# Performance work log

Hardware: AMD Instinct MI355X
Metric: run time of the kernel (lower is better)

The kernel has to match this reference:

```python
import jax, jax.numpy as jnp
import numpy as np

DIM = 1024
HEADS = 16
WINDOW = 5
B, S = 2, 2048
EPS = 1e-5


def setup_inputs() -> dict:
    key = jax.random.key(0)
    ks = jax.random.split(key, 12)
    d = DIM
    sc = lambda n: 1.0 / np.sqrt(n)
    return {
        "x": jax.random.normal(ks[0], (B, S, d), dtype=jnp.float32),
        "w_in": jax.random.normal(ks[1], (3 * d, d), dtype=jnp.float32) * sc(d),
        "b_in": jnp.zeros((3 * d,), dtype=jnp.float32),
        "w_out": jax.random.normal(ks[2], (d, d), dtype=jnp.float32) * sc(d),
        "b_out": jnp.zeros((d,), dtype=jnp.float32),
        "ln1_g": jnp.ones((d,), dtype=jnp.float32),
        "ln1_b": jnp.zeros((d,), dtype=jnp.float32),
        "ln2_g": jnp.ones((d,), dtype=jnp.float32),
        "ln2_b": jnp.zeros((d,), dtype=jnp.float32),
        "w1": jax.random.normal(ks[3], (4 * d, d), dtype=jnp.float32) * sc(d),
        "b1": jnp.zeros((4 * d,), dtype=jnp.float32),
        "w2": jax.random.normal(ks[4], (d, 4 * d), dtype=jnp.float32) * sc(4 * d),
        "b2": jnp.zeros((d,), dtype=jnp.float32),
    }


def _layernorm(x, g, b):
    mu = jnp.mean(x, axis=-1, keepdims=True)
    var = jnp.mean((x - mu) ** 2, axis=-1, keepdims=True)
    return (x - mu) * jax.lax.rsqrt(var + EPS) * g + b


def reference(x, w_in, b_in, w_out, b_out, ln1_g, ln1_b, ln2_g, ln2_b, w1, b1, w2, b2):
    Bq, Sq, d = x.shape
    hd = d // HEADS
    # in-projection (torch MHA: qkv = x @ W_in^T + b_in)
    qkv = jnp.einsum('bsd,ed->bse', x, w_in) + b_in  # [B,S,3d]
    q, k, v = jnp.split(qkv, 3, axis=-1)
    q = q.reshape(Bq, Sq, HEADS, hd)
    k = k.reshape(Bq, Sq, HEADS, hd)
    v = v.reshape(Bq, Sq, HEADS, hd)
    scale = 1.0 / np.sqrt(hd)
    scores = jnp.einsum('bqhd,bkhd->bhqk', q, k) * scale  # [B,H,S,S]
    # local causal mask: row i attends to j in [i-window+1, i]
    i = jnp.arange(Sq)[:, None]
    j = jnp.arange(Sq)[None, :]
    allowed = (j <= i) & (j > i - WINDOW)
    scores = jnp.where(allowed, scores, jnp.float32(-jnp.inf))
    probs = jax.nn.softmax(scores, axis=-1)
    attn = jnp.einsum('bhqk,bkhd->bqhd', probs, v).reshape(Bq, Sq, d)
    attn = jnp.einsum('bsd,ed->bse', attn, w_out) + b_out
    x1 = _layernorm(x + attn, ln1_g, ln1_b)
    h = jax.nn.gelu(jnp.einsum('bsd,ed->bse', x1, w1) + b1, approximate=False)
    mlp = jnp.einsum('bse,de->bsd', h, w2) + b2
    return _layernorm(x1 + mlp, ln2_g, ln2_b)
```

## Files before the change

### kernel.cpp

```cpp
#include <hip/hip_runtime.h>
#include <hip/hip_bf16.h>
#include <math.h>

typedef __hip_bfloat16 bf16;
typedef __attribute__((ext_vector_type(8))) short bf16x8;
typedef __attribute__((ext_vector_type(4))) float f32x4;

#define GPTR(p) ((const __attribute__((address_space(1))) void*)(p))
#define LPTR(p) ((__attribute__((address_space(3))) void*)(p))

__device__ __forceinline__ float b2f(short s) {
  unsigned int u = ((unsigned int)(unsigned short)s) << 16;
  float f; __builtin_memcpy(&f, &u, 4); return f;
}

__global__ __launch_bounds__(256) void cvt_all(
    const float* __restrict__ x,    const float* __restrict__ w_in,
    const float* __restrict__ w_out,const float* __restrict__ w1,
    const float* __restrict__ w2,
    bf16* __restrict__ xb,   bf16* __restrict__ winb, bf16* __restrict__ woutb,
    bf16* __restrict__ w1b,  bf16* __restrict__ w2b)
{
  const int b = blockIdx.x;
  const float* in; bf16* out; int base;
  if      (b <  4096) { in = x;     out = xb;    base = 0; }
  else if (b <  7168) { in = w_in;  out = winb;  base = 4096; }
  else if (b <  8192) { in = w_out; out = woutb; base = 7168; }
  else if (b < 12288) { in = w1;    out = w1b;   base = 8192; }
  else                { in = w2;    out = w2b;   base = 12288; }
  const int i = ((b - base) * 256 + threadIdx.x) * 4;
  const float4 f = *(const float4*)(in + i);
  ushort4 u;
  u.x = __bfloat16_as_ushort(__float2bfloat16(f.x));
  u.y = __bfloat16_as_ushort(__float2bfloat16(f.y));
  u.z = __bfloat16_as_ushort(__float2bfloat16(f.z));
  u.w = __bfloat16_as_ushort(__float2bfloat16(f.w));
  *(ushort4*)(out + i) = u;
}

__device__ __forceinline__ float gelu_fast(float v) {
  const float u  = 1.5957691216f * (v + 0.044715f * v * v * v);
  const float e  = __expf(u);
  return v * e / (e + 1.0f);
}

template<int GELU, int RESID>
__global__ __launch_bounds__(256, 4) void gemm_bt(
    const bf16* __restrict__ A, int lda,
    const bf16* __restrict__ B, int ldb,
    const float* __restrict__ bias,
    const void* __restrict__ Rv, int ldr,
    bf16* __restrict__ C, int ldc, long czstride,
    int M, int N, int kchunk)
{
  __shared__ __align__(16) bf16 As[128 * 64];
  __shared__ __align__(16) bf16 Bs[128 * 64];

  const int t    = threadIdx.x;
  const int lane = t & 63;
  const int w    = t >> 6;
  const int wm   = w >> 1;
  const int wn   = w & 1;
  const int lr   = lane & 15;
  const int lq   = lane >> 4;
  const int m0   = blockIdx.y * 128;
  const int n0   = blockIdx.x * 128;
  const int kz   = blockIdx.z;

  A += (size_t)kz * kchunk;
  B += (size_t)kz * kchunk;
  C += (size_t)kz * czstride;

  f32x4 acc[4][4];
  #pragma unroll
  for (int mi = 0; mi < 4; ++mi)
    #pragma unroll
    for (int ni = 0; ni < 4; ++ni)
      acc[mi][ni] = (f32x4){0.f, 0.f, 0.f, 0.f};

  const int wbase = (t & ~63) * 8;

  for (int k0 = 0; k0 < kchunk; k0 += 64) {
    #pragma unroll
    for (int it = 0; it < 4; ++it) {
      const int c    = it * 256 + t;
      const int row  = c >> 3;
      const int csw  = ((c & 7) ^ (row & 7)) << 3;
      const bf16* ga = A + (size_t)(m0 + row) * lda + k0 + csw;
      const bf16* gb = B + (size_t)(n0 + row) * ldb + k0 + csw;
      __builtin_amdgcn_global_load_lds(GPTR(ga), LPTR(&As[it * 2048 + wbase]), 16, 0, 0);
      __builtin_amdgcn_global_load_lds(GPTR(gb), LPTR(&Bs[it * 2048 + wbase]), 16, 0, 0);
    }
    __syncthreads();

    #pragma unroll
    for (int ks = 0; ks < 2; ++ks) {
      const int swz = (((ks * 4 + lq) ^ (lr & 7)) << 3);
      bf16x8 af[4], bfr[4];
      #pragma unroll
      for (int mi = 0; mi < 4; ++mi)
        af[mi] = *(const bf16x8*)&As[(wm * 64 + mi * 16 + lr) * 64 + swz];
      #pragma unroll
      for (int ni = 0; ni < 4; ++ni)
        bfr[ni] = *(const bf16x8*)&Bs[(wn * 64 + ni * 16 + lr) * 64 + swz];
      #pragma unroll
      for (int mi = 0; mi < 4; ++mi)
        #pragma unroll
        for (int ni = 0; ni < 4; ++ni)
          acc[mi][ni] = __builtin_amdgcn_mfma_f32_16x16x32_bf16(af[mi], bfr[ni], acc[mi][ni], 0, 0, 0);
    }
    __syncthreads();
  }

  #pragma unroll
  for (int ni = 0; ni < 4; ++ni) {
    const int col = n0 + wn * 64 + ni * 16 + lr;
    const float bv = bias ? bias[col] : 0.f;
    #pragma unroll
    for (int mi = 0; mi < 4; ++mi) {
      const int rowb = m0 + wm * 64 + mi * 16 + lq * 4;
      #pragma unroll
      for (int i = 0; i < 4; ++i) {
        float v = acc[mi][ni][i] + bv;
        if (GELU) v = gelu_fast(v);
        if (RESID == 1) v += ((const float*)Rv)[(size_t)(rowb + i) * ldr + col];
        if (RESID == 2) v += __bfloat162float(((const bf16*)Rv)[(size_t)(rowb + i) * ldr + col]);
        C[(size_t)(rowb + i) * ldc + col] = __float2bfloat16(v);
      }
    }
  }
}

__global__ __launch_bounds__(256) void attn_win(bf16* __restrict__ qkv)
{
  const int lane = threadIdx.x & 63;
  const int tk   = blockIdx.x * 4 + (threadIdx.x >> 6);
  const int s    = tk & 2047;
  const int doff = (lane >> 2) * 64 + (lane & 3) * 16;

  const size_t row = (size_t)tk * 3072;

  bf16x8 qa = *(const bf16x8*)&qkv[row + doff];
  bf16x8 qb = *(const bf16x8*)&qkv[row + doff + 8];
  float qf[16];
  #pragma unroll
  for (int e = 0; e < 8; ++e) { qf[e] = b2f(qa[e]); qf[8 + e] = b2f(qb[e]); }

  const int W = (s + 1 < 5) ? (s + 1) : 5;
  float p[5];
  #pragma unroll
  for (int j = 0; j < 5; ++j) {
    const int jc = (j < W) ? j : 0;
    const size_t kr = row - (size_t)jc * 3072 + 1024;
    bf16x8 ka = *(const bf16x8*)&qkv[kr + doff];
    bf16x8 kb = *(const bf16x8*)&qkv[kr + doff + 8];
    float d = 0.f;
    #pragma unroll
    for (int e = 0; e < 8; ++e) d += qf[e] * b2f(ka[e]);
    #pragma unroll
    for (int e = 0; e < 8; ++e) d += qf[8 + e] * b2f(kb[e]);
    d += __shfl_xor(d, 1);
    d += __shfl_xor(d, 2);
    p[j] = (j < W) ? d * 0.125f : -1e30f;
  }

  float mx = fmaxf(fmaxf(fmaxf(p[0], p[1]), fmaxf(p[2], p[3])), p[4]);
  float sum = 0.f;
  #pragma unroll
  for (int j = 0; j < 5; ++j) { p[j] = __expf(p[j] - mx); sum += p[j]; }
  const float inv = 1.f / sum;

  float o[16];
  #pragma unroll
  for (int e = 0; e < 16; ++e) o[e] = 0.f;
  #pragma unroll
  for (int j = 0; j < 5; ++j) {
    const int jc = (j < W) ? j : 0;
    const size_t vr = row - (size_t)jc * 3072 + 2048;
    bf16x8 va = *(const bf16x8*)&qkv[vr + doff];
    bf16x8 vb = *(const bf16x8*)&qkv[vr + doff + 8];
    #pragma unroll
    for (int e = 0; e < 8; ++e) { o[e] += p[j] * b2f(va[e]); o[8 + e] += p[j] * b2f(vb[e]); }
  }

  bf16x8 oa, ob;
  #pragma unroll
  for (int e = 0; e < 8; ++e) {
    oa[e] = (short)__bfloat16_as_ushort(__float2bfloat16(o[e] * inv));
    ob[e] = (short)__bfloat16_as_ushort(__float2bfloat16(o[8 + e] * inv));
  }
  *(bf16x8*)&qkv[row + doff]     = oa;
  *(bf16x8*)&qkv[row + doff + 8] = ob;
}

template<int OUTF32, int RESBF16>
__global__ __launch_bounds__(256) void ln_fuse(
    const bf16* __restrict__ P0, const bf16* __restrict__ P1, int ldp,
    const void* __restrict__ Rv,
    const float* __restrict__ bias,
    const float* __restrict__ g, const float* __restrict__ bt,
    void* __restrict__ outv)
{
  const int tk   = blockIdx.x * 4 + (threadIdx.x >> 6);
  const int lane = threadIdx.x & 63;
  const size_t bp = (size_t)tk * ldp;
  const size_t bo = (size_t)tk * 1024;

  float v[16];
  float sum = 0.f;
  #pragma unroll
  for (int i = 0; i < 16; ++i) {
    const int e = i * 64 + lane;
    float t = __bfloat162float(P0[bp + e]) + __bfloat162float(P1[bp + e]) + bias[e];
    if (RESBF16) t += __bfloat162float(((const bf16*)Rv)[bo + e]);
    else         t += ((const float*)Rv)[bo + e];
    v[i] = t;
    sum += t;
  }
  #pragma unroll
  for (int d = 1; d < 64; d <<= 1) sum += __shfl_xor(sum, d);
  const float mu = sum * (1.f / 1024.f);

  float sq = 0.f;
  #pragma unroll
  for (int i = 0; i < 16; ++i) { const float dv = v[i] - mu; sq += dv * dv; }
  #pragma unroll
  for (int d = 1; d < 64; d <<= 1) sq += __shfl_xor(sq, d);
  const float rstd = rsqrtf(sq * (1.f / 1024.f) + 1e-5f);

  #pragma unroll
  for (int i = 0; i < 16; ++i) {
    const int e = i * 64 + lane;
    const float o = (v[i] - mu) * rstd * g[e] + bt[e];
    if (OUTF32) ((float*)outv)[bo + e] = o;
    else        ((bf16*)outv)[bo + e] = __float2bfloat16(o);
  }
}

extern "C" void kernel_launch(void* const* d_in, const int* in_sizes, int n_in,
                              void* d_out, int out_size, void* d_ws, size_t ws_size,
                              hipStream_t stream)
{
  const float* x     = (const float*)d_in[0];
  const float* w_in  = (const float*)d_in[1];
  const float* b_in  = (const float*)d_in[2];
  const float* w_out = (const float*)d_in[3];
  const float* b_out = (const float*)d_in[4];
  const float* ln1_g = (const float*)d_in[5];
  const float* ln1_b = (const float*)d_in[6];
  const float* ln2_g = (const float*)d_in[7];
  const float* ln2_b = (const float*)d_in[8];
  const float* w1    = (const float*)d_in[9];
  const float* b1    = (const float*)d_in[10];
  const float* w2    = (const float*)d_in[11];
  const float* b2    = (const float*)d_in[12];
  float* out = (float*)d_out;

  char* ws = (char*)d_ws;
  bf16* qkv     = (bf16*)(ws);
  bf16* h       = (bf16*)(ws);
  bf16* x_b     = (bf16*)(ws + 33554432);
  bf16* x1_b    = (bf16*)(ws + 41943040);
  bf16* w1_b    = (bf16*)(ws + 50331648);
  bf16* w2_b    = (bf16*)(ws + 58720256);
  bf16* w_in_b  = (bf16*)(ws + 67108864);
  bf16* w_out_b = (bf16*)(ws + 73400320);
  bf16* P0      = x_b;
  bf16* P1      = w1_b;

  const dim3 blk(256);

  cvt_all<<<dim3(16384), blk, 0, stream>>>(x, w_in, w_out, w1, w2,
                                           x_b, w_in_b, w_out_b, w1_b, w2_b);

  gemm_bt<0,0><<<dim3(24, 32, 1), blk, 0, stream>>>(
      x_b, 1024, w_in_b, 1024, b_in, nullptr, 0, qkv, 3072, 0, 4096, 3072, 1024);
  attn_win<<<dim3(1024), blk, 0, stream>>>(qkv);
  gemm_bt<0,0><<<dim3(8, 32, 2), blk, 0, stream>>>(
      qkv, 3072, w_out_b, 1024, nullptr, nullptr, 0,
      qkv + 1024, 3072, 1024, 4096, 1024, 512);
  ln_fuse<0,0><<<dim3(1024), blk, 0, stream>>>(
      qkv + 1024, qkv + 2048, 3072, x, b_out, ln1_g, ln1_b, x1_b);
  gemm_bt<1,0><<<dim3(32, 32, 1), blk, 0, stream>>>(
      x1_b, 1024, w1_b, 1024, b1, nullptr, 0, h, 4096, 0, 4096, 4096, 1024);
  gemm_bt<0,0><<<dim3(8, 32, 2), blk, 0, stream>>>(
      h, 4096, w2_b, 4096, nullptr, nullptr, 0,
      P0, 1024, 8388608, 4096, 1024, 2048);
  ln_fuse<1,1><<<dim3(1024), blk, 0, stream>>>(
      P0, P1, 1024, x1_b, b2, ln2_g, ln2_b, out);
}
```

Measured before the change: 274.8 us.

## Remap GEMM blocks per XCD for L2 locality and vectorize layernorm loads

```diff
diff --git a/kernel.cpp b/kernel.cpp
--- a/kernel.cpp
+++ b/kernel.cpp
@@ -44,17 +44,25 @@
   return v * e / (e + 1.0f);
 }
 
-template<int GELU, int RESID>
+template<int GELU, int X, int Y, int Z>
 __global__ __launch_bounds__(256, 4) void gemm_bt(
     const bf16* __restrict__ A, int lda,
     const bf16* __restrict__ B, int ldb,
     const float* __restrict__ bias,
-    const void* __restrict__ Rv, int ldr,
     bf16* __restrict__ C, int ldc, long czstride,
-    int M, int N, int kchunk)
+    int kchunk)
 {
   __shared__ __align__(16) bf16 As[128 * 64];
   __shared__ __align__(16) bf16 Bs[128 * 64];
+
+  const int b  = blockIdx.x;
+  const int c  = b & 7;
+  const int i  = b >> 3;
+  const int xt = i % X;
+  const int r  = i / X;
+  const int yz = c * ((Y * Z) / 8) + r;
+  const int yt = yz % Y;
+  const int kz = yz / Y;
 
   const int t    = threadIdx.x;
   const int lane = t & 63;
@@ -63,9 +71,8 @@
   const int wn   = w & 1;
   const int lr   = lane & 15;
   const int lq   = lane >> 4;
-  const int m0   = blockIdx.y * 128;
-  const int n0   = blockIdx.x * 128;
-  const int kz   = blockIdx.z;
+  const int m0   = yt * 128;
+  const int n0   = xt * 128;
 
   A += (size_t)kz * kchunk;
   B += (size_t)kz * kchunk;
@@ -83,9 +90,9 @@
   for (int k0 = 0; k0 < kchunk; k0 += 64) {
     #pragma unroll
     for (int it = 0; it < 4; ++it) {
-      const int c    = it * 256 + t;
-      const int row  = c >> 3;
-      const int csw  = ((c & 7) ^ (row & 7)) << 3;
+      const int cc   = it * 256 + t;
+      const int row  = cc >> 3;
+      const int csw  = ((cc & 7) ^ (row & 7)) << 3;
       const bf16* ga = A + (size_t)(m0 + row) * lda + k0 + csw;
       const bf16* gb = B + (size_t)(n0 + row) * ldb + k0 + csw;
       __builtin_amdgcn_global_load_lds(GPTR(ga), LPTR(&As[it * 2048 + wbase]), 16, 0, 0);
@@ -120,12 +127,10 @@
     for (int mi = 0; mi < 4; ++mi) {
       const int rowb = m0 + wm * 64 + mi * 16 + lq * 4;
       #pragma unroll
-      for (int i = 0; i < 4; ++i) {
-        float v = acc[mi][ni][i] + bv;
+      for (int i2 = 0; i2 < 4; ++i2) {
+        float v = acc[mi][ni][i2] + bv;
         if (GELU) v = gelu_fast(v);
-        if (RESID == 1) v += ((const float*)Rv)[(size_t)(rowb + i) * ldr + col];
-        if (RESID == 2) v += __bfloat162float(((const bf16*)Rv)[(size_t)(rowb + i) * ldr + col]);
-        C[(size_t)(rowb + i) * ldc + col] = __float2bfloat16(v);
+        C[(size_t)(rowb + i2) * ldc + col] = __float2bfloat16(v);
       }
     }
   }
@@ -203,17 +208,21 @@
 {
   const int tk   = blockIdx.x * 4 + (threadIdx.x >> 6);
   const int lane = threadIdx.x & 63;
-  const size_t bp = (size_t)tk * ldp;
-  const size_t bo = (size_t)tk * 1024;
+  const int e0   = lane * 16;
+  const size_t bp = (size_t)tk * ldp + e0;
+  const size_t bo = (size_t)tk * 1024 + e0;
+
+  bf16x8 p0a = *(const bf16x8*)&P0[bp], p0b = *(const bf16x8*)&P0[bp + 8];
+  bf16x8 p1a = *(const bf16x8*)&P1[bp], p1b = *(const bf16x8*)&P1[bp + 8];
 
   float v[16];
   float sum = 0.f;
   #pragma unroll
   for (int i = 0; i < 16; ++i) {
-    const int e = i * 64 + lane;
-    float t = __bfloat162float(P0[bp + e]) + __bfloat162float(P1[bp + e]) + bias[e];
-    if (RESBF16) t += __bfloat162float(((const bf16*)Rv)[bo + e]);
-    else         t += ((const float*)Rv)[bo + e];
+    float t = (i < 8 ? b2f(p0a[i]) + b2f(p1a[i]) : b2f(p0b[i - 8]) + b2f(p1b[i - 8]))
+              + bias[e0 + i];
+    if (RESBF16) t += __bfloat162float(((const bf16*)Rv)[bo + i]);
+    else         t += ((const float*)Rv)[bo + i];
     v[i] = t;
     sum += t;
   }
@@ -228,12 +237,21 @@
   for (int d = 1; d < 64; d <<= 1) sq += __shfl_xor(sq, d);
   const float rstd = rsqrtf(sq * (1.f / 1024.f) + 1e-5f);
 
-  #pragma unroll
-  for (int i = 0; i < 16; ++i) {
-    const int e = i * 64 + lane;
-    const float o = (v[i] - mu) * rstd * g[e] + bt[e];
-    if (OUTF32) ((float*)outv)[bo + e] = o;
-    else        ((bf16*)outv)[bo + e] = __float2bfloat16(o);
+  if (OUTF32) {
+    float* op = (float*)outv;
+    #pragma unroll
+    for (int i = 0; i < 16; ++i)
+      op[bo + i] = (v[i] - mu) * rstd * g[e0 + i] + bt[e0 + i];
+  } else {
+    bf16x8 oa, ob;
+    #pragma unroll
+    for (int i = 0; i < 16; ++i) {
+      const float o = (v[i] - mu) * rstd * g[e0 + i] + bt[e0 + i];
+      if (i < 8) oa[i] = (short)__bfloat16_as_ushort(__float2bfloat16(o));
+      else       ob[i - 8] = (short)__bfloat16_as_ushort(__float2bfloat16(o));
+    }
+    *(bf16x8*)&((bf16*)outv)[bo]     = oa;
+    *(bf16x8*)&((bf16*)outv)[bo + 8] = ob;
   }
 }
 
@@ -273,19 +291,17 @@
   cvt_all<<<dim3(16384), blk, 0, stream>>>(x, w_in, w_out, w1, w2,
                                            x_b, w_in_b, w_out_b, w1_b, w2_b);
 
-  gemm_bt<0,0><<<dim3(24, 32, 1), blk, 0, stream>>>(
-      x_b, 1024, w_in_b, 1024, b_in, nullptr, 0, qkv, 3072, 0, 4096, 3072, 1024);
+  gemm_bt<0,24,32,1><<<dim3(768), blk, 0, stream>>>(
+      x_b, 1024, w_in_b, 1024, b_in, qkv, 3072, 0, 1024);
   attn_win<<<dim3(1024), blk, 0, stream>>>(qkv);
-  gemm_bt<0,0><<<dim3(8, 32, 2), blk, 0, stream>>>(
-      qkv, 3072, w_out_b, 1024, nullptr, nullptr, 0,
-      qkv + 1024, 3072, 1024, 4096, 1024, 512);
+  gemm_bt<0,8,32,2><<<dim3(512), blk, 0, stream>>>(
+      qkv, 3072, w_out_b, 1024, nullptr, qkv + 1024, 3072, 1024, 512);
   ln_fuse<0,0><<<dim3(1024), blk, 0, stream>>>(
       qkv + 1024, qkv + 2048, 3072, x, b_out, ln1_g, ln1_b, x1_b);
-  gemm_bt<1,0><<<dim3(32, 32, 1), blk, 0, stream>>>(
-      x1_b, 1024, w1_b, 1024, b1, nullptr, 0, h, 4096, 0, 4096, 4096, 1024);
-  gemm_bt<0,0><<<dim3(8, 32, 2), blk, 0, stream>>>(
-      h, 4096, w2_b, 4096, nullptr, nullptr, 0,
-      P0, 1024, 8388608, 4096, 1024, 2048);
+  gemm_bt<1,32,32,1><<<dim3(1024), blk, 0, stream>>>(
+      x1_b, 1024, w1_b, 1024, b1, h, 4096, 0, 1024);
+  gemm_bt<0,8,32,2><<<dim3(512), blk, 0, stream>>>(
+      h, 4096, w2_b, 4096, nullptr, P0, 1024, 8388608, 2048);
   ln_fuse<1,1><<<dim3(1024), blk, 0, stream>>>(
       P0, P1, 1024, x1_b, b2, ln2_g, ln2_b, out);
 }
```

Measured after the change: 280.5 us. 2.1% more time.
